# Kernel tuning notes

Hardware: AMD Instinct MI355X
Metric: run time of the kernel (lower is better)

Reference implementation:

```python
import jax, jax.numpy as jnp
import numpy as np
from jax import lax

# Resolved Optuna hyperparameters
NPOINTS = (512, 256, 128)
RADII = (0.2, 0.4, 0.8)
KS = (32, 32, 32)
BN_EPS = 1e-5


def _fps_single(pts, npoint):
    """Farthest point sampling on one cloud. pts: (N,3) -> (npoint,) int32."""
    N = pts.shape[0]
    def step(carry, _):
        dists, last = carry
        d = jnp.sum((pts - pts[last]) ** 2, axis=-1)
        dists = jnp.minimum(dists, d)
        nxt = jnp.argmax(dists).astype(jnp.int32)
        return (dists, nxt), last
    init = (jnp.full((N,), 1e10, pts.dtype), jnp.int32(0))
    (_, _), idx = lax.scan(step, init, None, length=npoint)
    return idx


def _set_abstraction(xyz, feat, W, b, radius, k, npoint):
    """xyz: (B,N,3), feat: (B,N,C_in) -> new_xyz (B,S,3), new_feat (B,S,C_out)."""
    B, N, _ = xyz.shape
    fps_idx = jax.vmap(lambda p: _fps_single(p, npoint))(xyz)          # (B,S)
    new_xyz = jax.vmap(lambda x, i: x[i])(xyz, fps_idx)                # (B,S,3)
    # ball query: squared distances centers -> all points
    d2 = jnp.sum((new_xyz[:, :, None, :] - xyz[:, None, :, :]) ** 2, axis=-1)  # (B,S,N)
    valid = d2 <= radius * radius
    ar = jnp.arange(N, dtype=jnp.int32)
    gi = jnp.where(valid, ar[None, None, :], N)                        # invalid -> N
    gi = jnp.sort(gi, axis=-1)[:, :, :k]                               # first k in index order
    first = gi[:, :, :1]
    gi = jnp.where(gi == N, first, gi)                                 # pad with first valid (center itself)
    g_xyz = jax.vmap(lambda x, i: x[i])(xyz, gi)                       # (B,S,k,3)
    rel = g_xyz - new_xyz[:, :, None, :]
    g_feat = jax.vmap(lambda x, i: x[i])(feat, gi)                     # (B,S,k,C_in)
    h = jnp.concatenate([rel, g_feat], axis=-1)                        # (B,S,k,3+C_in)
    h = jax.nn.relu(jnp.einsum('bskc,co->bsko', h, W) + b)
    return new_xyz, jnp.max(h, axis=2)                                 # max-pool over group


def _bn(x, g, b):
    # nn.BatchNorm1d training-mode forward (batch statistics, biased var)
    m = x.mean(axis=0)
    v = x.var(axis=0)
    return (x - m) * lax.rsqrt(v + BN_EPS) * g + b


def setup_inputs() -> dict:
    key = jax.random.key(0)
    ks = jax.random.split(key, 8)
    def w(k, i, o):
        return (jax.random.normal(k, (i, o), jnp.float32) / np.sqrt(i)).astype(jnp.float32)
    return dict(
        points=jax.random.uniform(ks[0], (16, 4096, 3), jnp.float32),
        W1=w(ks[1], 3 + 3, 64),   b1=jnp.zeros((64,), jnp.float32),
        W2=w(ks[2], 64 + 3, 128), b2=jnp.zeros((128,), jnp.float32),
        W3=w(ks[3], 128 + 3, 256), b3=jnp.zeros((256,), jnp.float32),
        fc1_w=w(ks[4], 256, 256), fc1_b=jnp.zeros((256,), jnp.float32),
        fc2_w=w(ks[5], 256, 128), fc2_b=jnp.zeros((128,), jnp.float32),
        fc3_w=w(ks[6], 128, 12),  fc3_b=jnp.zeros((12,), jnp.float32),
        bn1_g=jnp.ones((256,), jnp.float32), bn1_b=jnp.zeros((256,), jnp.float32),
        bn2_g=jnp.ones((128,), jnp.float32), bn2_b=jnp.zeros((128,), jnp.float32),
    )


def reference(points, W1, b1, W2, b2, W3, b3, fc1_w, fc1_b, fc2_w, fc2_b,
              fc3_w, fc3_b, bn1_g, bn1_b, bn2_g, bn2_b):
    B = points.shape[0]
    xyz, feat = points, points
    for (W, bb, r, k, s) in ((W1, b1, RADII[0], KS[0], NPOINTS[0]),
                             (W2, b2, RADII[1], KS[1], NPOINTS[1]),
                             (W3, b3, RADII[2], KS[2], NPOINTS[2])):
        xyz, feat = _set_abstraction(xyz, feat, W, bb, r, k, s)
    f = jnp.max(feat, axis=1)                                          # (B, ch3)
    x = jax.nn.relu(_bn(f @ fc1_w + fc1_b, bn1_g, bn1_b))              # dropout: eval-mode identity
    x = jax.nn.relu(_bn(x @ fc2_w + fc2_b, bn2_g, bn2_b))
    x = x @ fc3_w + fc3_b
    return x.reshape(B, 4, 3)
```

## Files before the change

### kernel.cpp

```cpp
#include <hip/hip_runtime.h>
#include <hip/hip_bf16.h>


#define B_SZ 16

template<int CTRL>
__device__ __forceinline__ float dpp_mv(float v) {
    const int i = __float_as_int(v);
    const int r = __builtin_amdgcn_update_dpp(i, i, CTRL, 0xf, 0xf, false);
    return __int_as_float(r);
}

__device__ __forceinline__ float wave_max_f32(float x) {
    float v = x;
    v = fmaxf(v, dpp_mv<0x111>(v));
    v = fmaxf(v, dpp_mv<0x112>(v));
    v = fmaxf(v, dpp_mv<0x114>(v));
    v = fmaxf(v, dpp_mv<0x118>(v));
    v = fmaxf(v, dpp_mv<0x142>(v));
    v = fmaxf(v, dpp_mv<0x143>(v));
    return __uint_as_float(__builtin_amdgcn_readlane(__float_as_uint(v), 63));
}

__device__ __forceinline__ float read_lane_f32(float v, int l) {
    return __uint_as_float(__builtin_amdgcn_readlane(__float_as_uint(v), l));
}

template<int N, int NPOINT, int BLOCK, int S0, int S1, bool FIRST>
__device__ __forceinline__ void fps_body(
    const float* __restrict__ xyz,
    float* __restrict__ newxyz,
    float* __restrict__ dstate,
    const int b)
{
    constexpr int P  = N / BLOCK;
    constexpr int NW = BLOCK / 64;
    constexpr int O0 = FIRST ? 0 : S0;
    __shared__ float4 part[2][NW];
    __shared__ float  outb[(S1 - O0) * 3];

    const int tid = threadIdx.x;
    const int lane = tid & 63, w = tid >> 6;
    const float* xb = xyz + (size_t)b * N * 3;

    float px[P], py[P], pz[P], dd[P];
    const int base = tid * P;
#pragma unroll
    for (int i = 0; i < P; i++) {
        px[i] = xb[(base + i) * 3 + 0];
        py[i] = xb[(base + i) * 3 + 1];
        pz[i] = xb[(base + i) * 3 + 2];
    }
    float lx, ly, lz;
    if (FIRST) {
#pragma unroll
        for (int i = 0; i < P; i++) dd[i] = 1e10f;
        lx = xb[0]; ly = xb[1]; lz = xb[2];
        if (tid == 0) { outb[0] = lx; outb[1] = ly; outb[2] = lz; }
    } else {
#pragma unroll
        for (int i = 0; i < P; i++) dd[i] = dstate[((size_t)b * P + i) * BLOCK + tid];
        const float* c = newxyz + ((size_t)b * NPOINT + (S0 - 1)) * 3;
        lx = c[0]; ly = c[1]; lz = c[2];
    }

    for (int s = S0; s < S1; s++) {
        float bv = -1.0f, bx = 0.0f, by = 0.0f, bz = 0.0f;
#pragma unroll
        for (int i = 0; i < P; i++) {
            const float dx = px[i] - lx, dy = py[i] - ly, dz = pz[i] - lz;
            const float d2 = __fadd_rn(__fadd_rn(__fmul_rn(dx, dx), __fmul_rn(dy, dy)),
                                       __fmul_rn(dz, dz));
            const float nd = fminf(dd[i], d2);
            dd[i] = nd;
            const bool gt = nd > bv;
            bv = gt ? nd : bv;
            bx = gt ? px[i] : bx;
            by = gt ? py[i] : by;
            bz = gt ? pz[i] : bz;
        }
        const float wmax = wave_max_f32(bv);
        const unsigned long long mset = __ballot(bv == wmax);
        const int li = __ffsll(mset) - 1;
        const int buf = s & 1;
        if (lane == li) part[buf][w] = make_float4(bv, bx, by, bz);
        __syncthreads();
        float cv = -1.0f;
#pragma unroll
        for (int q = 0; q < NW; q++) {
            const float4 pq = part[buf][q];
            const bool gt = pq.x > cv;
            cv = gt ? pq.x : cv;
            lx = gt ? pq.y : lx;
            ly = gt ? pq.z : ly;
            lz = gt ? pq.w : lz;
        }
        if (tid == 0) {
            const int t = (s - O0) * 3;
            outb[t + 0] = lx; outb[t + 1] = ly; outb[t + 2] = lz;
        }
    }
    __syncthreads();
    if (S1 < NPOINT) {
#pragma unroll
        for (int i = 0; i < P; i++)
            dstate[((size_t)b * P + i) * BLOCK + tid] = dd[i];
    }
    float* o = newxyz + ((size_t)b * NPOINT + O0) * 3;
    for (int t = tid; t < (S1 - O0) * 3; t += BLOCK) o[t] = outb[t];
}

template<int N, int NPOINT, int BLOCK, int S0, int S1, bool FIRST>
__global__ __launch_bounds__(BLOCK) void fps_kernel(
    const float* __restrict__ xyz, float* __restrict__ newxyz,
    float* __restrict__ dstate)
{
    fps_body<N, NPOINT, BLOCK, S0, S1, FIRST>(xyz, newxyz, dstate, blockIdx.x);
}

template<int N, int NPOINT>
__device__ __forceinline__ void fps_wave_body(
    const float* __restrict__ xyz,
    float* __restrict__ newxyz,
    const int b, const int lane)
{
    constexpr int P = N / 64;
    const float* xb = xyz + (size_t)b * N * 3;

    float px[P], py[P], pz[P], dd[P];
    const int base = lane * P;
#pragma unroll
    for (int i = 0; i < P; i++) {
        px[i] = xb[(base + i) * 3 + 0];
        py[i] = xb[(base + i) * 3 + 1];
        pz[i] = xb[(base + i) * 3 + 2];
        dd[i] = 1e10f;
    }
#pragma unroll
    for (int i = 0; i < P; i++) {
        asm volatile("" : "+v"(px[i]), "+v"(py[i]), "+v"(pz[i]));
    }
    float lx = xb[0], ly = xb[1], lz = xb[2];
    if (lane == 0) {
        float* o = newxyz + (size_t)b * NPOINT * 3;
        o[0] = lx; o[1] = ly; o[2] = lz;
    }

    for (int s = 1; s < NPOINT; s++) {
        float bv = -1.0f, bx = 0.0f, by = 0.0f, bz = 0.0f;
#pragma unroll
        for (int i = 0; i < P; i++) {
            const float dx = px[i] - lx, dy = py[i] - ly, dz = pz[i] - lz;
            const float d2 = __fadd_rn(__fadd_rn(__fmul_rn(dx, dx), __fmul_rn(dy, dy)),
                                       __fmul_rn(dz, dz));
            const float nd = fminf(dd[i], d2);
            dd[i] = nd;
            const bool gt = nd > bv;
            bv = gt ? nd : bv;
            bx = gt ? px[i] : bx;
            by = gt ? py[i] : by;
            bz = gt ? pz[i] : bz;
        }
        const float wmax = wave_max_f32(bv);
        const unsigned long long mset = __ballot(bv == wmax);
        const int li = __ffsll(mset) - 1;
        lx = read_lane_f32(bx, li);
        ly = read_lane_f32(by, li);
        lz = read_lane_f32(bz, li);
        if (lane == 0) {
            float* o = newxyz + ((size_t)b * NPOINT + s) * 3;
            o[0] = lx; o[1] = ly; o[2] = lz;
        }
    }
}

template<int N, int S, int CF, int COUT, int R, bool AMAX>
__device__ __forceinline__ void sa_body(
    const float* __restrict__ xyz,
    const float* __restrict__ feat,
    const float* __restrict__ cent,
    const float* __restrict__ W,
    const float* __restrict__ bias,
    float* __restrict__ outf,
    const float r2, const int s, const int b, const int lane,
    int* __restrict__ gi, float* __restrict__ h)
{
    constexpr int K    = 32;
    constexpr int JT   = 16;
    constexpr int CIN  = CF + 3;
    constexpr int CINP = (CIN + 3) & ~3;
    constexpr int C4   = CIN & ~3;

    const float* xb = xyz  + (size_t)b * N * 3;
    const float* fb = feat + (size_t)b * N * CF;
    const float cx = cent[((size_t)b * S + s) * 3 + 0];
    const float cy = cent[((size_t)b * S + s) * 3 + 1];
    const float cz = cent[((size_t)b * S + s) * 3 + 2];

    constexpr int RND = N / 256;
    int total = 0, g0 = 0;
    for (int r0 = 0; r0 < RND; r0++) {
        if (total >= K) break;
        float xs[4], ys[4], zs[4];
#pragma unroll
        for (int c4 = 0; c4 < 4; c4++) {
            const int p = (r0 * 4 + c4) * 64 + lane;
            xs[c4] = xb[p * 3 + 0];
            ys[c4] = xb[p * 3 + 1];
            zs[c4] = xb[p * 3 + 2];
        }
#pragma unroll
        for (int c4 = 0; c4 < 4; c4++) {
            const int p = (r0 * 4 + c4) * 64 + lane;
            const float dx = xs[c4] - cx, dy = ys[c4] - cy, dz = zs[c4] - cz;
            const float d2 = __fadd_rn(__fadd_rn(__fmul_rn(dx, dx), __fmul_rn(dy, dy)),
                                       __fmul_rn(dz, dz));
            const bool v = (d2 <= r2);
            const unsigned long long bal = __ballot(v);
            if (total == 0 && bal != 0ull) g0 = (r0 * 4 + c4) * 64 + (__ffsll(bal) - 1);
            const int pos = total + __popcll(bal & ((1ull << lane) - 1ull));
            if (v && pos < K) gi[pos] = p;
            total += __popcll(bal);
        }
    }
    if (lane == 0 && total < K) {
        for (int q = total; q < K; q++) gi[q] = g0;
    }
    __syncthreads();

    float m[R];
#pragma unroll
    for (int r = 0; r < R; r++) m[r] = -1e30f;

    for (int pass = 0; pass < K / JT; pass++) {
        for (int jj = 0; jj < JT; jj++) {
            const int idx = gi[pass * JT + jj];
            for (int c = lane; c < CIN; c += 64) {
                float val;
                if (c < 3) {
                    const float cc = (c == 0) ? cx : ((c == 1) ? cy : cz);
                    val = xb[idx * 3 + c] - cc;
                } else {
                    val = fb[(size_t)idx * CF + (c - 3)];
                }
                h[jj * CINP + c] = val;
            }
        }
        __syncthreads();

        float acc[JT][R];
#pragma unroll
        for (int jj = 0; jj < JT; jj++)
#pragma unroll
            for (int r = 0; r < R; r++) acc[jj][r] = 0.0f;

        const float* wp = W + lane;
        int c = 0;
        for (; c < C4; c += 4) {
            float wv[4][R];
#pragma unroll
            for (int q = 0; q < 4; q++)
#pragma unroll
                for (int r = 0; r < R; r++)
                    wv[q][r] = wp[(size_t)(c + q) * COUT + r * 64];
#pragma unroll
            for (int jj = 0; jj < JT; jj++) {
                const float4 hv = *(const float4*)&h[jj * CINP + c];
#pragma unroll
                for (int r = 0; r < R; r++) {
                    acc[jj][r] = fmaf(hv.x, wv[0][r], acc[jj][r]);
                    acc[jj][r] = fmaf(hv.y, wv[1][r], acc[jj][r]);
                    acc[jj][r] = fmaf(hv.z, wv[2][r], acc[jj][r]);
                    acc[jj][r] = fmaf(hv.w, wv[3][r], acc[jj][r]);
                }
            }
        }
        for (; c < CIN; c++) {
            float wv[R];
#pragma unroll
            for (int r = 0; r < R; r++) wv[r] = wp[(size_t)c * COUT + r * 64];
#pragma unroll
            for (int jj = 0; jj < JT; jj++) {
                const float hv = h[jj * CINP + c];
#pragma unroll
                for (int r = 0; r < R; r++)
                    acc[jj][r] = fmaf(hv, wv[r], acc[jj][r]);
            }
        }
#pragma unroll
        for (int jj = 0; jj < JT; jj++)
#pragma unroll
            for (int r = 0; r < R; r++) m[r] = fmaxf(m[r], acc[jj][r]);
        __syncthreads();
    }

#pragma unroll
    for (int r = 0; r < R; r++) {
        const int o = r * 64 + lane;
        const float val = fmaxf(bias[o] + m[r], 0.0f);
        if (AMAX) {
            atomicMax((unsigned*)&outf[(size_t)b * COUT + o], __float_as_uint(val));
        } else {
            outf[((size_t)b * S + s) * COUT + o] = val;
        }
    }
}

template<int N, int S, int CF, int COUT, int R, bool AMAX>
__global__ __launch_bounds__(64) void sa_kernel(
    const float* __restrict__ xyz, const float* __restrict__ feat,
    const float* __restrict__ cent, const float* __restrict__ W,
    const float* __restrict__ bias, float* __restrict__ outf, const float r2)
{
    constexpr int CINP = (CF + 3 + 3) & ~3;
    __shared__ int   gi[32];
    __shared__ float h[16 * CINP];
    sa_body<N, S, CF, COUT, R, AMAX>(xyz, feat, cent, W, bias, outf, r2,
                                     blockIdx.x, blockIdx.y, threadIdx.x, gi, h);
}

template<int N, int S, int CF, int COUT, int R, int SCNT>
__global__ __launch_bounds__(512) void fused_fps1b_sa_kernel(
    const float* __restrict__ fxyz, float* __restrict__ fnew,
    float* __restrict__ fdd,
    const float* __restrict__ xyz, const float* __restrict__ feat,
    const float* __restrict__ cent, const float* __restrict__ W,
    const float* __restrict__ bias, float* __restrict__ outf, const float r2)
{
    constexpr int CINP = (CF + 3 + 3) & ~3;
    if (blockIdx.x < B_SZ) {
        __builtin_amdgcn_s_setprio(3);
        fps_body<4096, 512, 512, 256, 512, false>(fxyz, fnew, fdd, blockIdx.x);
    } else {
        __shared__ int   gi_s[8][32];
        __shared__ float h_s[8][16 * CINP];
        const int w = threadIdx.x >> 6, lane = threadIdx.x & 63;
        const int widx = (blockIdx.x - B_SZ) * 8 + w;
        const int b = widx / SCNT, s = widx % SCNT;
        sa_body<N, S, CF, COUT, R, false>(xyz, feat, cent, W, bias, outf, r2,
                                          s, b, lane, gi_s[w], h_s[w]);
    }
}

template<int NF, int NPF, int N, int S, int CF, int COUT, int R,
         int SOFF, int SCNT>
__global__ __launch_bounds__(64) void fused_fps_sa_kernel(
    const float* __restrict__ fxyz,
    float* __restrict__ fnew,
    const float* __restrict__ xyz, const float* __restrict__ feat,
    const float* __restrict__ cent, const float* __restrict__ W,
    const float* __restrict__ bias, float* __restrict__ outf, const float r2)
{
    constexpr int CINP = (CF + 3 + 3) & ~3;
    if (blockIdx.x < B_SZ) {
        __builtin_amdgcn_s_setprio(3);
        fps_wave_body<NF, NPF>(fxyz, fnew, blockIdx.x, threadIdx.x);
    } else {
        __shared__ int   gi[32];
        __shared__ float h[16 * CINP];
        const int i = blockIdx.x - B_SZ;
        sa_body<N, S, CF, COUT, R, false>(xyz, feat, cent, W, bias, outf, r2,
                                          SOFF + i % SCNT, i / SCNT,
                                          threadIdx.x, gi, h);
    }
}

__global__ __launch_bounds__(64) void fc1_kernel(
    const float* __restrict__ f,
    const float* __restrict__ w,
    const float* __restrict__ bias,
    float* __restrict__ x1h)
{
    const int r = blockIdx.x >> 2;
    const int o = (blockIdx.x & 3) * 64 + threadIdx.x;
    const float* fr = f + r * 256;
    float acc = bias[o];
    for (int c = 0; c < 256; c += 4) {
        acc = fmaf(fr[c + 0], w[(size_t)(c + 0) * 256 + o], acc);
        acc = fmaf(fr[c + 1], w[(size_t)(c + 1) * 256 + o], acc);
        acc = fmaf(fr[c + 2], w[(size_t)(c + 2) * 256 + o], acc);
        acc = fmaf(fr[c + 3], w[(size_t)(c + 3) * 256 + o], acc);
    }
    x1h[r * 256 + o] = acc;
}

__global__ __launch_bounds__(256) void head2_kernel(
    const float* __restrict__ x1h,
    const float* __restrict__ fc2_w, const float* __restrict__ fc2_b,
    const float* __restrict__ fc3_w, const float* __restrict__ fc3_b,
    const float* __restrict__ bn1_g, const float* __restrict__ bn1_b,
    const float* __restrict__ bn2_g, const float* __restrict__ bn2_b,
    float* __restrict__ out)
{
    __shared__ float x1[16 * 257];
    __shared__ float x2[16 * 129];
    const int tid = threadIdx.x;

    for (int idx = tid; idx < 16 * 256; idx += 256) {
        const int r = idx >> 8, c = idx & 255;
        x1[r * 257 + c] = x1h[idx];
    }
    __syncthreads();
    {
        const int o = tid;
        float v[16];
#pragma unroll
        for (int r = 0; r < 16; r++) v[r] = x1[r * 257 + o];
        float m = 0.0f;
#pragma unroll
        for (int r = 0; r < 16; r++) m += v[r];
        m *= (1.0f / 16.0f);
        float var = 0.0f;
#pragma unroll
        for (int r = 0; r < 16; r++) { const float d = v[r] - m; var += d * d; }
        var *= (1.0f / 16.0f);
        const float sc = bn1_g[o] / sqrtf(var + 1e-5f);
        const float sh = bn1_b[o];
#pragma unroll
        for (int r = 0; r < 16; r++)
            x1[r * 257 + o] = fmaxf((v[r] - m) * sc + sh, 0.0f);
    }
    __syncthreads();
    {
        const int r = tid >> 4, g = tid & 15;
        float acc[8];
#pragma unroll
        for (int i = 0; i < 8; i++) acc[i] = fc2_b[g * 8 + i];
        const float* wrow = fc2_w + g * 8;
        for (int c = 0; c < 256; c++) {
            const float fv = x1[r * 257 + c];
            const float4* w4 = (const float4*)(wrow + (size_t)c * 128);
#pragma unroll
            for (int q = 0; q < 2; q++) {
                const float4 wv = w4[q];
                acc[q * 4 + 0] = fmaf(fv, wv.x, acc[q * 4 + 0]);
                acc[q * 4 + 1] = fmaf(fv, wv.y, acc[q * 4 + 1]);
                acc[q * 4 + 2] = fmaf(fv, wv.z, acc[q * 4 + 2]);
                acc[q * 4 + 3] = fmaf(fv, wv.w, acc[q * 4 + 3]);
            }
        }
#pragma unroll
        for (int i = 0; i < 8; i++) x2[r * 129 + g * 8 + i] = acc[i];
    }
    __syncthreads();
    if (tid < 128) {
        const int o = tid;
        float v[16];
#pragma unroll
        for (int r = 0; r < 16; r++) v[r] = x2[r * 129 + o];
        float m = 0.0f;
#pragma unroll
        for (int r = 0; r < 16; r++) m += v[r];
        m *= (1.0f / 16.0f);
        float var = 0.0f;
#pragma unroll
        for (int r = 0; r < 16; r++) { const float d = v[r] - m; var += d * d; }
        var *= (1.0f / 16.0f);
        const float sc = bn2_g[o] / sqrtf(var + 1e-5f);
        const float sh = bn2_b[o];
#pragma unroll
        for (int r = 0; r < 16; r++)
            x2[r * 129 + o] = fmaxf((v[r] - m) * sc + sh, 0.0f);
    }
    __syncthreads();
    if (tid < 192) {
        const int r = tid / 12, j = tid - r * 12;
        float acc = fc3_b[j];
        for (int c = 0; c < 128; c++)
            acc = fmaf(x2[r * 129 + c], fc3_w[c * 12 + j], acc);
        out[r * 12 + j] = acc;
    }
}

extern "C" void kernel_launch(void* const* d_in, const int* in_sizes, int n_in,
                              void* d_out, int out_size, void* d_ws, size_t ws_size,
                              hipStream_t stream) {
    const float* points = (const float*)d_in[0];
    const float* W1     = (const float*)d_in[1];
    const float* b1     = (const float*)d_in[2];
    const float* W2     = (const float*)d_in[3];
    const float* b2     = (const float*)d_in[4];
    const float* W3     = (const float*)d_in[5];
    const float* b3     = (const float*)d_in[6];
    const float* fc1_w  = (const float*)d_in[7];
    const float* fc1_b  = (const float*)d_in[8];
    const float* fc2_w  = (const float*)d_in[9];
    const float* fc2_b  = (const float*)d_in[10];
    const float* fc3_w  = (const float*)d_in[11];
    const float* fc3_b  = (const float*)d_in[12];
    const float* bn1_g  = (const float*)d_in[13];
    const float* bn1_b  = (const float*)d_in[14];
    const float* bn2_g  = (const float*)d_in[15];
    const float* bn2_b  = (const float*)d_in[16];
    float* out = (float*)d_out;

    float* ws   = (float*)d_ws;
    float* nx1  = ws;
    float* f1   = nx1 + 24576;
    float* nx2  = f1  + 524288;
    float* f2   = nx2 + 12288;
    float* nx3  = f2  + 524288;
    float* fmx  = nx3 + 6144;
    float* fdd  = fmx + 4096;
    float* x1h  = fdd + 65536;

    fps_kernel<4096, 512, 512, 1, 256, true><<<B_SZ, 512, 0, stream>>>(
        points, nx1, fdd);
    fused_fps1b_sa_kernel<4096, 512, 3, 64, 1, 256>
        <<<B_SZ + 512, 512, 0, stream>>>(
        points, nx1, fdd, points, points, nx1, W1, b1, f1, (float)(0.2 * 0.2));
    fused_fps_sa_kernel<512, 256, 4096, 512, 3, 64, 1, 256, 256>
        <<<B_SZ + 256 * B_SZ, 64, 0, stream>>>(
        nx1, nx2, points, points, nx1, W1, b1, f1, (float)(0.2 * 0.2));
    fused_fps_sa_kernel<256, 128, 512, 256, 64, 128, 2, 0, 256>
        <<<B_SZ + 256 * B_SZ, 64, 0, stream>>>(
        nx2, nx3, nx1, f1, nx2, W2, b2, f2, (float)(0.4 * 0.4));
    hipMemsetAsync(fmx, 0, 16 * 256 * sizeof(float), stream);
    sa_kernel<256, 128, 128, 256, 4, true><<<dim3(128, B_SZ), 64, 0, stream>>>(
        nx2, f2, nx3, W3, b3, fmx, (float)(0.8 * 0.8));
    fc1_kernel<<<64, 64, 0, stream>>>(fmx, fc1_w, fc1_b, x1h);
    head2_kernel<<<1, 256, 0, stream>>>(x1h, fc2_w, fc2_b, fc3_w, fc3_b,
                                        bn1_g, bn1_b, bn2_g, bn2_b, out);
}
```

Baseline: 709.1 us.

## Split first-level FPS into finer chunks overlapped with SA1 groups; fold memset into kernel

The first-level farthest point sampling is now split into four stages of 128 centroids instead of two of 256. Each later stage runs in the same launch as set-abstraction work on the centroids already produced, so the serial FPS overlaps with more of the grouping and MLP work. The separate memset of the global max buffer is dropped, and the FPS blocks of a later fused kernel zero that buffer instead. This adds two kernel launches and more FPS restart overhead, and it relies on the fdd distance state being carried correctly between stages.

```diff
diff --git a/kernel.cpp b/kernel.cpp
--- a/kernel.cpp
+++ b/kernel.cpp
@@ -319,40 +319,45 @@
                                      blockIdx.x, blockIdx.y, threadIdx.x, gi, h);
 }
 
-template<int N, int S, int CF, int COUT, int R, int SCNT>
-__global__ __launch_bounds__(512) void fused_fps1b_sa_kernel(
+template<int S0, int S1, int SOFF, int SCNT>
+__global__ __launch_bounds__(512) void fused_fps1_sa_kernel(
     const float* __restrict__ fxyz, float* __restrict__ fnew,
     float* __restrict__ fdd,
     const float* __restrict__ xyz, const float* __restrict__ feat,
     const float* __restrict__ cent, const float* __restrict__ W,
     const float* __restrict__ bias, float* __restrict__ outf, const float r2)
 {
-    constexpr int CINP = (CF + 3 + 3) & ~3;
+    constexpr int CINP = 8;
     if (blockIdx.x < B_SZ) {
         __builtin_amdgcn_s_setprio(3);
-        fps_body<4096, 512, 512, 256, 512, false>(fxyz, fnew, fdd, blockIdx.x);
+        fps_body<4096, 512, 512, S0, S1, false>(fxyz, fnew, fdd, blockIdx.x);
     } else {
         __shared__ int   gi_s[8][32];
         __shared__ float h_s[8][16 * CINP];
         const int w = threadIdx.x >> 6, lane = threadIdx.x & 63;
         const int widx = (blockIdx.x - B_SZ) * 8 + w;
-        const int b = widx / SCNT, s = widx % SCNT;
-        sa_body<N, S, CF, COUT, R, false>(xyz, feat, cent, W, bias, outf, r2,
-                                          s, b, lane, gi_s[w], h_s[w]);
+        const int b = widx / SCNT, s = SOFF + widx % SCNT;
+        sa_body<4096, 512, 3, 64, 1, false>(xyz, feat, cent, W, bias, outf, r2,
+                                            s, b, lane, gi_s[w], h_s[w]);
     }
 }
 
 template<int NF, int NPF, int N, int S, int CF, int COUT, int R,
-         int SOFF, int SCNT>
+         int SOFF, int SCNT, bool ZERO>
 __global__ __launch_bounds__(64) void fused_fps_sa_kernel(
     const float* __restrict__ fxyz,
     float* __restrict__ fnew,
     const float* __restrict__ xyz, const float* __restrict__ feat,
     const float* __restrict__ cent, const float* __restrict__ W,
-    const float* __restrict__ bias, float* __restrict__ outf, const float r2)
+    const float* __restrict__ bias, float* __restrict__ outf,
+    float* __restrict__ fmx, const float r2)
 {
     constexpr int CINP = (CF + 3 + 3) & ~3;
     if (blockIdx.x < B_SZ) {
+        if (ZERO) {
+            ((float4*)fmx)[blockIdx.x * 64 + threadIdx.x] =
+                make_float4(0.f, 0.f, 0.f, 0.f);
+        }
         __builtin_amdgcn_s_setprio(3);
         fps_wave_body<NF, NPF>(fxyz, fnew, blockIdx.x, threadIdx.x);
     } else {
@@ -504,18 +509,21 @@
     float* fdd  = fmx + 4096;
     float* x1h  = fdd + 65536;
 
-    fps_kernel<4096, 512, 512, 1, 256, true><<<B_SZ, 512, 0, stream>>>(
+    const float r21 = (float)(0.2 * 0.2);
+    fps_kernel<4096, 512, 512, 1, 128, true><<<B_SZ, 512, 0, stream>>>(
         points, nx1, fdd);
-    fused_fps1b_sa_kernel<4096, 512, 3, 64, 1, 256>
-        <<<B_SZ + 512, 512, 0, stream>>>(
-        points, nx1, fdd, points, points, nx1, W1, b1, f1, (float)(0.2 * 0.2));
-    fused_fps_sa_kernel<512, 256, 4096, 512, 3, 64, 1, 256, 256>
+    fused_fps1_sa_kernel<128, 256, 0, 128><<<B_SZ + 256, 512, 0, stream>>>(
+        points, nx1, fdd, points, points, nx1, W1, b1, f1, r21);
+    fused_fps1_sa_kernel<256, 384, 128, 128><<<B_SZ + 256, 512, 0, stream>>>(
+        points, nx1, fdd, points, points, nx1, W1, b1, f1, r21);
+    fused_fps1_sa_kernel<384, 512, 256, 128><<<B_SZ + 256, 512, 0, stream>>>(
+        points, nx1, fdd, points, points, nx1, W1, b1, f1, r21);
+    fused_fps_sa_kernel<512, 256, 4096, 512, 3, 64, 1, 384, 128, true>
+        <<<B_SZ + 128 * B_SZ, 64, 0, stream>>>(
+        nx1, nx2, points, points, nx1, W1, b1, f1, fmx, r21);
+    fused_fps_sa_kernel<256, 128, 512, 256, 64, 128, 2, 0, 256, false>
         <<<B_SZ + 256 * B_SZ, 64, 0, stream>>>(
-        nx1, nx2, points, points, nx1, W1, b1, f1, (float)(0.2 * 0.2));
-    fused_fps_sa_kernel<256, 128, 512, 256, 64, 128, 2, 0, 256>
-        <<<B_SZ + 256 * B_SZ, 64, 0, stream>>>(
-        nx2, nx3, nx1, f1, nx2, W2, b2, f2, (float)(0.4 * 0.4));
-    hipMemsetAsync(fmx, 0, 16 * 256 * sizeof(float), stream);
+        nx2, nx3, nx1, f1, nx2, W2, b2, f2, fmx, (float)(0.4 * 0.4));
     sa_kernel<256, 128, 128, 256, 4, true><<<dim3(128, B_SZ), 64, 0, stream>>>(
         nx2, f2, nx3, W3, b3, fmx, (float)(0.8 * 0.8));
     fc1_kernel<<<64, 64, 0, stream>>>(fmx, fc1_w, fc1_b, x1h);
```

Result: no change. 710.6 us (+0.2%).
